# Kernel tuning notes

Hardware: AMD Instinct MI355X
Metric: run time of the kernel (lower is better)

Reference implementation:

```python
import jax, jax.numpy as jnp
import numpy as np

NEG_SLOPE = 0.1
NUM_HEADS = 16
ATT0, ATT1 = 64, 64
FOCUS = 3

def lrelu(x):
    return jnp.where(x >= 0, x, NEG_SLOPE * x)

def adaptive_pool_sum(x, a0, a1):
    # adaptive max pool + adaptive avg pool (exact windows since h%a0==0, w%a1==0)
    B, C, h, w = x.shape
    f0, f1 = h // a0, w // a1
    xr = x.reshape(B, C, a0, f0, a1, f1)
    return xr.max(axis=(3, 5)) + xr.mean(axis=(3, 5))

def upsample_bilinear_ac(x, H, W):
    # bilinear upsample with align_corners=True, matching nn.Upsample
    B, C, h, w = x.shape
    def grid(n_out, n_in):
        t = jnp.arange(n_out, dtype=x.dtype) * ((n_in - 1) / (n_out - 1))
        i0 = jnp.clip(jnp.floor(t).astype(jnp.int32), 0, n_in - 2)
        return i0, t - i0.astype(x.dtype)
    y0, wy = grid(H, h)
    x0, wx = grid(W, w)
    wy = wy[None, None, :, None]
    r = x[:, :, y0, :] * (1 - wy) + x[:, :, y0 + 1, :] * wy
    return r[:, :, :, x0] * (1 - wx) + r[:, :, :, x0 + 1] * wx

def _forward(input1, input2, w_in, b_in, w_v, b_v, scale_param, pos1, pos2):
    B, C, W, H = input1.shape
    N = ATT0 * ATT1
    HD = C // NUM_HEADS
    # conv2input: 1x1 conv dim//2 -> dim (channels differ)
    input2 = jnp.einsum('oc,bchw->bohw', w_in, input2) + b_in[None, :, None, None]
    p1 = adaptive_pool_sum(input1, ATT0, ATT1)  # (B,C,64,64)
    p2 = adaptive_pool_sum(input2, ATT0, ATT1)
    q = p1.reshape(B, C, N).transpose(0, 2, 1)  # (B,N,C)
    t2 = p2.reshape(B, C, N).transpose(0, 2, 1)
    q = lrelu(q + pos1)
    k = lrelu(t2 + pos2)
    v = t2
    scale = jax.nn.softplus(scale_param)  # (1,1,C)
    q = q / scale
    k = k / scale
    def focus(t):
        n = jnp.linalg.norm(t, axis=-1, keepdims=True)
        tp = t ** FOCUS
        return n / jnp.linalg.norm(tp, axis=-1, keepdims=True) * tp
    q = focus(q)
    k = focus(k)
    # head split is head-major: C -> (num_heads, head_dim)
    qh = q.reshape(B, N, NUM_HEADS, HD).transpose(0, 2, 1, 3)  # (B,h,N,d)
    kh = k.reshape(B, N, NUM_HEADS, HD).transpose(0, 2, 1, 3)
    vh = v.reshape(B, N, NUM_HEADS, HD).transpose(0, 2, 1, 3)
    # kv-first linear attention: (k^T N^-.5) @ (v N^-.5) = k^T v / N
    kv = jnp.einsum('bhnd,bhne->bhde', kh, vh) / N  # (B,h,d,d)
    x = jnp.einsum('bhnd,bhde->bhne', qh, kv)       # (B,h,N,d)
    x = x.transpose(0, 1, 3, 2).reshape(B, C, N)     # (B,h,d,N) -> (B,C,N)
    # per-head 1x1 conv + leaky relu on v
    v4 = vh.reshape(B * NUM_HEADS, ATT0, ATT1, HD)
    vc = lrelu(jnp.einsum('bxyd,od->boxy', v4, w_v) + b_v[None, :, None, None])
    x = x + vc.reshape(B, C, N)
    attn = x.reshape(B, C, ATT0, ATT1)
    attn = upsample_bilinear_ac(attn, W, H)
    return jax.nn.sigmoid(attn)

def setup_inputs():
    key = jax.random.key(0)
    ks = jax.random.split(key, 6)
    dim, half, hd, N = 512, 256, 32, ATT0 * ATT1
    return {
        'input1': jax.random.normal(ks[0], (8, dim, 128, 128), jnp.float32),
        'input2': jax.random.normal(ks[1], (8, half, 128, 128), jnp.float32),
        'w_in': jax.random.normal(ks[2], (dim, half), jnp.float32) * 0.05,
        'b_in': jnp.zeros((dim,), jnp.float32),
        'w_v': jax.random.normal(ks[3], (hd, hd), jnp.float32) * 0.1,
        'b_v': jnp.zeros((hd,), jnp.float32),
        'scale_param': jnp.zeros((1, 1, dim), jnp.float32),  # nn.Parameter init zeros
        'pos1': jax.random.normal(ks[4], (1, N, dim), jnp.float32) * 0.02,
        'pos2': jax.random.normal(ks[5], (1, N, dim), jnp.float32) * 0.02,
    }

def reference(input1, input2, w_in, b_in, w_v, b_v, scale_param, pos1, pos2):
    return _forward(input1, input2, w_in, b_in, w_v, b_v, scale_param, pos1, pos2)
```

## Files before the change

### kernel.cpp

```cpp
#include <hip/hip_runtime.h>
#include <math.h>

#define NEG 0.1f

typedef __attribute__((ext_vector_type(8))) short short8;
typedef __attribute__((ext_vector_type(4))) float f32x4;

__device__ __forceinline__ float lrelu(float x){ return x >= 0.f ? x : NEG*x; }

__device__ __forceinline__ unsigned short f2bf(float f){
    unsigned u = __float_as_uint(f);
    return (unsigned short)((u + 0x7FFFu + ((u>>16)&1u)) >> 16);
}
__device__ __forceinline__ unsigned pk2(float lo, float hi){
    return (unsigned)f2bf(lo) | ((unsigned)f2bf(hi) << 16);
}
__device__ __forceinline__ float bflo(unsigned u){ return __uint_as_float(u << 16); }
__device__ __forceinline__ float bfhi(unsigned u){ return __uint_as_float(u & 0xFFFF0000u); }

__global__ __launch_bounds__(256) void k_pool1(const float* __restrict__ in1, unsigned short* __restrict__ p1t){
    __shared__ float s[64*68];
    const int b = blockIdx.z, c0 = blockIdx.y*64, pt = blockIdx.x;
    const int y = pt >> 2, xg = pt & 3;
    const int tid = threadIdx.x;
    #pragma unroll
    for (int it = 0; it < 16; ++it){
        int idx = it*256 + tid;
        int cl = idx >> 6, p = idx & 63;
        int r = p >> 5, xx = p & 31;
        float g = in1[((size_t)(b*512 + c0 + cl)*128 + 2*y + r)*128 + xg*32 + xx];
        s[cl*68 + (xx>>1)*4 + r*2 + (xx&1)] = g;
    }
    __syncthreads();
    const int og = tid & 15, j = tid >> 4;
    float out[4];
    #pragma unroll
    for (int ci = 0; ci < 4; ++ci){
        float4 v = *(const float4*)&s[(og*4+ci)*68 + j*4];
        float m = fmaxf(fmaxf(v.x,v.y), fmaxf(v.z,v.w));
        out[ci] = m + (v.x+v.y+v.z+v.w)*0.25f;
    }
    int n = y*64 + xg*16 + j;
    uint2 d; d.x = pk2(out[0],out[1]); d.y = pk2(out[2],out[3]);
    *(uint2*)&p1t[(size_t)(b*4096 + n)*512 + c0 + og*4] = d;
}

__global__ __launch_bounds__(256) void k_convpool(const float* __restrict__ in2, const float* __restrict__ w_in,
                                                  const float* __restrict__ b_in, unsigned short* __restrict__ p2t){
    __shared__ unsigned As[128*33];
    __shared__ unsigned Bs[128*32];
    const int b = blockIdx.z, o0 = blockIdx.y*128;
    const int y = blockIdx.x >> 1, xg = blockIdx.x & 1;
    const int tid = threadIdx.x;
    const int lane = tid & 63, w = tid >> 6;
    const int col = lane & 15, q = lane >> 4;

    f32x4 acc[2][8];
    #pragma unroll
    for (int mt=0; mt<2; ++mt)
        #pragma unroll
        for (int nt=0; nt<8; ++nt) acc[mt][nt] = (f32x4){0.f,0.f,0.f,0.f};

    const int a_o8 = tid >> 3;
    const int a_kg = tid & 7;
    const int b_c4 = tid & 15, b_r = (tid>>4)&1, b_kg = tid>>5;
    const int b_n = b_r*64 + b_c4*4;

    for (int kb = 0; kb < 4; ++kb){
        __syncthreads();
        #pragma unroll
        for (int pass=0; pass<4; ++pass){
            int o = pass*32 + a_o8;
            const float* src = &w_in[(size_t)(o0+o)*256 + kb*64 + a_kg*8];
            float4 v0 = *(const float4*)src;
            float4 v1 = *(const float4*)(src+4);
            uint4 d;
            d.x = pk2(v0.x, v0.y); d.y = pk2(v0.z, v0.w);
            d.z = pk2(v1.x, v1.y); d.w = pk2(v1.z, v1.w);
            *(uint4*)&As[o*32 + ((a_kg ^ ((o>>1)&7))<<2)] = d;
        }
        float r[8][4];
        #pragma unroll
        for (int kk=0; kk<8; ++kk){
            int k = kb*64 + b_kg*8 + kk;
            float4 v = *(const float4*)&in2[((size_t)(b*256 + k)*128 + 2*y + b_r)*128 + xg*64 + b_c4*4];
            r[kk][0]=v.x; r[kk][1]=v.y; r[kk][2]=v.z; r[kk][3]=v.w;
        }
        #pragma unroll
        for (int i=0; i<4; ++i){
            int n = b_n + i;
            uint4 d;
            d.x = pk2(r[0][i], r[1][i]); d.y = pk2(r[2][i], r[3][i]);
            d.z = pk2(r[4][i], r[5][i]); d.w = pk2(r[6][i], r[7][i]);
            *(uint4*)&Bs[n*32 + ((b_kg ^ ((n>>1)&7))<<2)] = d;
        }
        __syncthreads();
        #pragma unroll
        for (int ks=0; ks<2; ++ks){
            int g = ks*4 + q;
            short8 af[2], bf[8];
            #pragma unroll
            for (int mt=0; mt<2; ++mt){
                int m = w*32 + mt*16 + col;
                af[mt] = *(const short8*)&As[m*32 + ((g ^ ((m>>1)&7))<<2)];
            }
            #pragma unroll
            for (int nt=0; nt<8; ++nt){
                int n = nt*16 + col;
                bf[nt] = *(const short8*)&Bs[n*32 + ((g ^ ((n>>1)&7))<<2)];
            }
            #pragma unroll
            for (int mt=0; mt<2; ++mt)
                #pragma unroll
                for (int nt=0; nt<8; ++nt)
                    acc[mt][nt] = __builtin_amdgcn_mfma_f32_16x16x32_bf16(af[mt], bf[nt], acc[mt][nt], 0,0,0);
        }
    }
    __syncthreads();
    float* outs = (float*)As;
    #pragma unroll
    for (int mt=0; mt<2; ++mt){
        #pragma unroll
        for (int nt=0; nt<4; ++nt){
            #pragma unroll
            for (int reg=0; reg<4; ++reg){
                float a = acc[mt][nt][reg], bb = acc[mt][nt+4][reg];
                float mx = fmaxf(a, bb), sm = a + bb;
                float mx2 = fmaxf(mx, __shfl_xor(mx, 1));
                float sm2 = sm + __shfl_xor(sm, 1);
                if ((lane & 1) == 0){
                    int p = nt*8 + (col>>1);
                    int o = w*32 + mt*16 + q*4 + reg;
                    outs[o*33 + p] = mx2 + sm2*0.25f;
                }
            }
        }
    }
    __syncthreads();
    const int o4 = tid & 31, pp = tid >> 5;
    #pragma unroll
    for (int pass=0; pass<4; ++pass){
        int p = pass*8 + pp;
        int n = y*64 + xg*32 + p;
        float v0 = outs[(o4*4+0)*33 + p] + 2.0f*b_in[o0+o4*4+0];
        float v1 = outs[(o4*4+1)*33 + p] + 2.0f*b_in[o0+o4*4+1];
        float v2 = outs[(o4*4+2)*33 + p] + 2.0f*b_in[o0+o4*4+2];
        float v3 = outs[(o4*4+3)*33 + p] + 2.0f*b_in[o0+o4*4+3];
        uint2 d; d.x = pk2(v0,v1); d.y = pk2(v2,v3);
        *(uint2*)&p2t[(size_t)(b*4096 + n)*512 + o0 + o4*4] = d;
    }
}

__global__ __launch_bounds__(256) void k_rows(unsigned* __restrict__ p1u, const unsigned* __restrict__ p2u,
                                              const float* __restrict__ pos1, const float* __restrict__ pos2,
                                              const float* __restrict__ scale_param, unsigned* __restrict__ kfu){
    const int n = blockIdx.x, b = blockIdx.y;
    const int tid = threadIdx.x;
    const size_t baseu = (size_t)(b*4096 + n)*256;
    const int c0 = tid*2;
    __shared__ float red[4][4];
    unsigned u1 = p1u[baseu + tid];
    unsigned u2 = p2u[baseu + tid];
    float2 po1 = *(const float2*)&pos1[n*512 + c0];
    float2 po2 = *(const float2*)&pos2[n*512 + c0];
    float2 scv = *(const float2*)&scale_param[c0];
    float qv[2], kv_[2];
    float pq2=0.f, pq6=0.f, pk2_=0.f, pk6=0.f;
    {
        float sp0 = scv.x, sp1 = scv.y;
        float inv0 = 1.0f/(fmaxf(sp0,0.f) + log1pf(expf(-fabsf(sp0))));
        float inv1 = 1.0f/(fmaxf(sp1,0.f) + log1pf(expf(-fabsf(sp1))));
        float q0 = lrelu(bflo(u1) + po1.x) * inv0;
        float q1 = lrelu(bfhi(u1) + po1.y) * inv1;
        float k0 = lrelu(bflo(u2) + po2.x) * inv0;
        float k1 = lrelu(bfhi(u2) + po2.y) * inv1;
        qv[0]=q0; qv[1]=q1; kv_[0]=k0; kv_[1]=k1;
        float a;
        a = q0*q0; pq2 += a; pq6 += a*a*a;
        a = q1*q1; pq2 += a; pq6 += a*a*a;
        a = k0*k0; pk2_ += a; pk6 += a*a*a;
        a = k1*k1; pk2_ += a; pk6 += a*a*a;
    }
    #pragma unroll
    for (int off = 32; off > 0; off >>= 1){
        pq2 += __shfl_xor(pq2, off);
        pq6 += __shfl_xor(pq6, off);
        pk2_ += __shfl_xor(pk2_, off);
        pk6 += __shfl_xor(pk6, off);
    }
    int wave = tid >> 6;
    if ((tid & 63) == 0){ red[wave][0]=pq2; red[wave][1]=pq6; red[wave][2]=pk2_; red[wave][3]=pk6; }
    __syncthreads();
    float sq2 = red[0][0]+red[1][0]+red[2][0]+red[3][0];
    float sq6 = red[0][1]+red[1][1]+red[2][1]+red[3][1];
    float sk2 = red[0][2]+red[1][2]+red[2][2]+red[3][2];
    float sk6 = red[0][3]+red[1][3]+red[2][3]+red[3][3];
    float fq = sqrtf(sq2/sq6);
    float fk = sqrtf(sk2/sk6);
    p1u[baseu + tid] = pk2(qv[0]*qv[0]*qv[0]*fq, qv[1]*qv[1]*qv[1]*fq);
    kfu[baseu + tid] = pk2(kv_[0]*kv_[0]*kv_[0]*fk, kv_[1]*kv_[1]*kv_[1]*fk);
}

__global__ __launch_bounds__(256) void k_kv(const unsigned* __restrict__ kfu, const unsigned* __restrict__ p2u,
                                            float* __restrict__ kv){
    __shared__ float ks[512], vs[512];
    const int nc = blockIdx.x, h = blockIdx.y, b = blockIdx.z;
    const int tid = threadIdx.x;
    const int d = tid >> 3, eb = (tid & 7) * 4;
    const int nn_ld = tid >> 4, cp = tid & 15;
    float acc[4] = {0.f,0.f,0.f,0.f};
    for (int s = 0; s < 16; ++s){
        int n0 = nc*256 + s*16;
        size_t g = (size_t)(b*4096 + n0 + nn_ld)*256 + h*16 + cp;
        unsigned ku = kfu[g], vu = p2u[g];
        ks[nn_ld*32 + cp*2]   = bflo(ku);
        ks[nn_ld*32 + cp*2+1] = bfhi(ku);
        vs[nn_ld*32 + cp*2]   = bflo(vu);
        vs[nn_ld*32 + cp*2+1] = bfhi(vu);
        __syncthreads();
        #pragma unroll
        for (int nn = 0; nn < 16; ++nn){
            float kd = ks[nn*32 + d];
            float4 vv = *(const float4*)&vs[nn*32 + eb];
            acc[0] += kd*vv.x; acc[1] += kd*vv.y; acc[2] += kd*vv.z; acc[3] += kd*vv.w;
        }
        __syncthreads();
    }
    float* dst = &kv[((size_t)(b*16 + h)*32 + d)*32 + eb];
    const float sc = 1.0f/4096.0f;
    atomicAdd(dst+0, acc[0]*sc);
    atomicAdd(dst+1, acc[1]*sc);
    atomicAdd(dst+2, acc[2]*sc);
    atomicAdd(dst+3, acc[3]*sc);
}

__global__ __launch_bounds__(256) void k_attn(const unsigned* __restrict__ qfu, const unsigned* __restrict__ p2u,
                                              const float* __restrict__ kv, const float* __restrict__ w_v,
                                              const float* __restrict__ b_v, unsigned short* __restrict__ attn){
    __shared__ float kvs[1024];
    __shared__ float wvsT[32*36];
    __shared__ float qsl[64*32];
    __shared__ float vsl[64*32];
    __shared__ float to[32*66];
    const int nt = blockIdx.x, h = blockIdx.y, b = blockIdx.z;
    const int tid = threadIdx.x;
    #pragma unroll
    for (int it = 0; it < 4; ++it){
        int i = it*256 + tid;
        kvs[i] = kv[(size_t)(b*16 + h)*1024 + i];
        int e_ = i >> 5, d_ = i & 31;
        wvsT[d_*36 + e_] = w_v[e_*32 + d_];
    }
    #pragma unroll
    for (int it = 0; it < 4; ++it){
        int i = it*256 + tid;
        int nn = i >> 4, cp = i & 15;
        size_t g = (size_t)(b*4096 + nt*64 + nn)*256 + h*16 + cp;
        unsigned qu = qfu[g], vu = p2u[g];
        qsl[nn*32 + cp*2]   = bflo(qu);
        qsl[nn*32 + cp*2+1] = bfhi(qu);
        vsl[nn*32 + cp*2]   = bflo(vu);
        vsl[nn*32 + cp*2+1] = bfhi(vu);
    }
    __syncthreads();
    const int e0 = (tid & 7)*4, ng = tid >> 3;
    float4 bv = make_float4(b_v[e0], b_v[e0+1], b_v[e0+2], b_v[e0+3]);
    #pragma unroll
    for (int half = 0; half < 2; ++half){
        int nn = ng + half*32;
        float xa[4] = {0.f,0.f,0.f,0.f}, va[4] = {0.f,0.f,0.f,0.f};
        #pragma unroll
        for (int dq = 0; dq < 8; ++dq){
            float4 q4 = *(const float4*)&qsl[nn*32 + dq*4];
            float4 v4 = *(const float4*)&vsl[nn*32 + dq*4];
            float qarr[4] = {q4.x,q4.y,q4.z,q4.w};
            float varr[4] = {v4.x,v4.y,v4.z,v4.w};
            #pragma unroll
            for (int l = 0; l < 4; ++l){
                int d = dq*4 + l;
                float4 kvv = *(const float4*)&kvs[d*32 + e0];
                float4 wvv = *(const float4*)&wvsT[d*36 + e0];
                xa[0] += qarr[l]*kvv.x; xa[1] += qarr[l]*kvv.y; xa[2] += qarr[l]*kvv.z; xa[3] += qarr[l]*kvv.w;
                va[0] += varr[l]*wvv.x; va[1] += varr[l]*wvv.y; va[2] += varr[l]*wvv.z; va[3] += varr[l]*wvv.w;
            }
        }
        to[(e0+0)*66 + nn] = xa[0] + lrelu(va[0] + bv.x);
        to[(e0+1)*66 + nn] = xa[1] + lrelu(va[1] + bv.y);
        to[(e0+2)*66 + nn] = xa[2] + lrelu(va[2] + bv.z);
        to[(e0+3)*66 + nn] = xa[3] + lrelu(va[3] + bv.w);
    }
    __syncthreads();
    const int cc = tid >> 3, n0 = (tid & 7)*8;
    uint4 d;
    d.x = pk2(to[cc*66+n0+0], to[cc*66+n0+1]);
    d.y = pk2(to[cc*66+n0+2], to[cc*66+n0+3]);
    d.z = pk2(to[cc*66+n0+4], to[cc*66+n0+5]);
    d.w = pk2(to[cc*66+n0+6], to[cc*66+n0+7]);
    *(uint4*)&attn[((size_t)(b*512) + h*32 + cc)*4096 + nt*64 + n0] = d;
}

__global__ __launch_bounds__(256) void k_up(const unsigned* __restrict__ attn_u, float* __restrict__ out){
    __shared__ float sA[18*65];
    const int qy = blockIdx.x;
    const int bc = blockIdx.y;
    const int tid = threadIdx.x;
    const int ybase = (qy*32*63)/127;
    const size_t sb = (size_t)bc*2048;
    for (int i = tid; i < 576; i += 256){
        int r = i >> 5, cu = i & 31;
        int ridx = ybase + r; if (ridx > 63) ridx = 63;
        unsigned u = attn_u[sb + ridx*32 + cu];
        sA[r*65 + cu*2]   = bflo(u);
        sA[r*65 + cu*2+1] = bfhi(u);
    }
    __syncthreads();
    const float rr = 63.0f/127.0f;
    const int ro = tid >> 3, cbase = tid & 7;
    const int yo = qy*32 + ro;
    float ty = yo * rr;
    int y0 = (int)ty; y0 = y0 > 62 ? 62 : y0;
    float wy = ty - (float)y0;
    const float* ra = &sA[(y0 - ybase)*65];
    const float* rb = ra + 65;
    float* orow = &out[((size_t)bc*128 + yo)*128];
    #pragma unroll
    for (int t = 0; t < 4; ++t){
        int xo0 = (cbase + t*8)*4;
        float4 o;
        float* op = (float*)&o;
        #pragma unroll
        for (int j = 0; j < 4; ++j){
            int xo = xo0 + j;
            float tx = xo * rr;
            int x0 = (int)tx; x0 = x0 > 62 ? 62 : x0;
            float wx = tx - (float)x0;
            float a00 = ra[x0], a01 = ra[x0+1];
            float a10 = rb[x0], a11 = rb[x0+1];
            float v = (a00*(1.f-wy) + a10*wy)*(1.f-wx) + (a01*(1.f-wy) + a11*wy)*wx;
            op[j] = 1.0f/(1.0f + expf(-v));
        }
        *(float4*)&orow[xo0] = o;
    }
}

extern "C" void kernel_launch(void* const* d_in, const int* in_sizes, int n_in,
                              void* d_out, int out_size, void* d_ws, size_t ws_size,
                              hipStream_t stream){
    const float* in1  = (const float*)d_in[0];
    const float* in2  = (const float*)d_in[1];
    const float* w_in = (const float*)d_in[2];
    const float* b_in = (const float*)d_in[3];
    const float* w_v  = (const float*)d_in[4];
    const float* b_v  = (const float*)d_in[5];
    const float* scp  = (const float*)d_in[6];
    const float* pos1 = (const float*)d_in[7];
    const float* pos2 = (const float*)d_in[8];
    float* out = (float*)d_out;
    char* ws  = (char*)d_ws;

    const size_t PBYTES = (size_t)8*4096*512*2;
    unsigned short* p1t  = (unsigned short*)ws;
    unsigned short* p2t  = (unsigned short*)(ws + PBYTES);
    unsigned short* kfoc = (unsigned short*)(ws + 2*PBYTES);
    float*          kvb  = (float*)(ws + 3*PBYTES);

    hipMemsetAsync(kvb, 0, (size_t)8*16*32*32*sizeof(float), stream);
    k_pool1   <<<dim3(256,8,8), 256, 0, stream>>>(in1, p1t);
    k_convpool<<<dim3(128,4,8), 256, 0, stream>>>(in2, w_in, b_in, p2t);
    k_rows    <<<dim3(4096,8),  256, 0, stream>>>((unsigned*)p1t, (const unsigned*)p2t, pos1, pos2, scp, (unsigned*)kfoc);
    k_kv      <<<dim3(16,16,8), 256, 0, stream>>>((const unsigned*)kfoc, (const unsigned*)p2t, kvb);
    k_attn    <<<dim3(64,16,8), 256, 0, stream>>>((const unsigned*)p1t, (const unsigned*)p2t, kvb, w_v, b_v, kfoc);
    k_up      <<<dim3(4,4096),  256, 0, stream>>>((const unsigned*)kfoc, out);
}
```

Measured before the change: 843.7 us.

## Rework pool1, row normalisation, kv reduction and pre-convert conv weights to bf16

Several kernels change at once. k_pool1 drops the shared-memory transpose and reads float2 pairs directly, writing 8 channels per thread. A new k_wprep kernel converts w_in to bf16 once, so k_convpool loads packed weights instead of converting them in every block. k_rows handles two rows per block with 4 channels per thread, and k_kv stages its whole 256-row chunk in shared memory as bf16 with a single sync. bf16 packing now uses the HIP intrinsic. The aim is fewer blocks, fewer barriers and wider memory accesses, at the cost of an extra launch and less coalesced pool reads.

```diff
diff --git a/kernel.cpp b/kernel.cpp
--- a/kernel.cpp
+++ b/kernel.cpp
@@ -1,4 +1,5 @@
 #include <hip/hip_runtime.h>
+#include <hip/hip_bf16.h>
 #include <math.h>
 
 #define NEG 0.1f
@@ -8,44 +9,48 @@
 
 __device__ __forceinline__ float lrelu(float x){ return x >= 0.f ? x : NEG*x; }
 
-__device__ __forceinline__ unsigned short f2bf(float f){
-    unsigned u = __float_as_uint(f);
-    return (unsigned short)((u + 0x7FFFu + ((u>>16)&1u)) >> 16);
-}
 __device__ __forceinline__ unsigned pk2(float lo, float hi){
-    return (unsigned)f2bf(lo) | ((unsigned)f2bf(hi) << 16);
+    __hip_bfloat162 h = __float22bfloat162_rn(make_float2(lo, hi));
+    union { __hip_bfloat162 h2; unsigned u; } cv; cv.h2 = h;
+    return cv.u;
 }
 __device__ __forceinline__ float bflo(unsigned u){ return __uint_as_float(u << 16); }
 __device__ __forceinline__ float bfhi(unsigned u){ return __uint_as_float(u & 0xFFFF0000u); }
 
-__global__ __launch_bounds__(256) void k_pool1(const float* __restrict__ in1, unsigned short* __restrict__ p1t){
-    __shared__ float s[64*68];
-    const int b = blockIdx.z, c0 = blockIdx.y*64, pt = blockIdx.x;
-    const int y = pt >> 2, xg = pt & 3;
-    const int tid = threadIdx.x;
-    #pragma unroll
-    for (int it = 0; it < 16; ++it){
-        int idx = it*256 + tid;
-        int cl = idx >> 6, p = idx & 63;
-        int r = p >> 5, xx = p & 31;
-        float g = in1[((size_t)(b*512 + c0 + cl)*128 + 2*y + r)*128 + xg*32 + xx];
-        s[cl*68 + (xx>>1)*4 + r*2 + (xx&1)] = g;
-    }
-    __syncthreads();
-    const int og = tid & 15, j = tid >> 4;
-    float out[4];
-    #pragma unroll
-    for (int ci = 0; ci < 4; ++ci){
-        float4 v = *(const float4*)&s[(og*4+ci)*68 + j*4];
-        float m = fmaxf(fmaxf(v.x,v.y), fmaxf(v.z,v.w));
-        out[ci] = m + (v.x+v.y+v.z+v.w)*0.25f;
-    }
-    int n = y*64 + xg*16 + j;
-    uint2 d; d.x = pk2(out[0],out[1]); d.y = pk2(out[2],out[3]);
-    *(uint2*)&p1t[(size_t)(b*4096 + n)*512 + c0 + og*4] = d;
-}
-
-__global__ __launch_bounds__(256) void k_convpool(const float* __restrict__ in2, const float* __restrict__ w_in,
+__global__ __launch_bounds__(256) void k_wprep(const float* __restrict__ w_in, unsigned* __restrict__ wbf_u){
+    int idx8 = (blockIdx.x*256 + threadIdx.x)*8;
+    float4 v0 = *(const float4*)&w_in[idx8];
+    float4 v1 = *(const float4*)&w_in[idx8+4];
+    uint4 d;
+    d.x = pk2(v0.x, v0.y); d.y = pk2(v0.z, v0.w);
+    d.z = pk2(v1.x, v1.y); d.w = pk2(v1.z, v1.w);
+    *(uint4*)&wbf_u[idx8>>1] = d;
+}
+
+__global__ __launch_bounds__(256) void k_pool1(const float* __restrict__ in1, unsigned* __restrict__ p1u){
+    const int y = blockIdx.x, cg = blockIdx.y, b = blockIdx.z;
+    const int tid = threadIdx.x;
+    const int x = tid & 63, w = tid >> 6;
+    const int cbase = cg*32 + w*8;
+    const float2* iv = (const float2*)in1;
+    float out[8];
+    #pragma unroll
+    for (int j = 0; j < 8; ++j){
+        int c = cbase + j;
+        size_t r0 = (size_t)(b*512 + c)*8192 + (2*y)*64 + x;
+        float2 a = iv[r0];
+        float2 bb = iv[r0 + 64];
+        float m = fmaxf(fmaxf(a.x,a.y), fmaxf(bb.x,bb.y));
+        out[j] = m + (a.x+a.y+bb.x+bb.y)*0.25f;
+    }
+    uint4 d;
+    d.x = pk2(out[0],out[1]); d.y = pk2(out[2],out[3]);
+    d.z = pk2(out[4],out[5]); d.w = pk2(out[6],out[7]);
+    int n = y*64 + x;
+    *(uint4*)&p1u[(size_t)(b*4096 + n)*256 + cg*16 + w*4] = d;
+}
+
+__global__ __launch_bounds__(256) void k_convpool(const float* __restrict__ in2, const unsigned* __restrict__ wbf_u,
                                                   const float* __restrict__ b_in, unsigned short* __restrict__ p2t){
     __shared__ unsigned As[128*33];
     __shared__ unsigned Bs[128*32];
@@ -71,12 +76,7 @@
         #pragma unroll
         for (int pass=0; pass<4; ++pass){
             int o = pass*32 + a_o8;
-            const float* src = &w_in[(size_t)(o0+o)*256 + kb*64 + a_kg*8];
-            float4 v0 = *(const float4*)src;
-            float4 v1 = *(const float4*)(src+4);
-            uint4 d;
-            d.x = pk2(v0.x, v0.y); d.y = pk2(v0.z, v0.w);
-            d.z = pk2(v1.x, v1.y); d.w = pk2(v1.z, v1.w);
+            uint4 d = *(const uint4*)&wbf_u[((size_t)(o0+o)*256 + kb*64 + a_kg*8) >> 1];
             *(uint4*)&As[o*32 + ((a_kg ^ ((o>>1)&7))<<2)] = d;
         }
         float r[8][4];
@@ -154,32 +154,37 @@
 __global__ __launch_bounds__(256) void k_rows(unsigned* __restrict__ p1u, const unsigned* __restrict__ p2u,
                                               const float* __restrict__ pos1, const float* __restrict__ pos2,
                                               const float* __restrict__ scale_param, unsigned* __restrict__ kfu){
-    const int n = blockIdx.x, b = blockIdx.y;
-    const int tid = threadIdx.x;
-    const size_t baseu = (size_t)(b*4096 + n)*256;
-    const int c0 = tid*2;
+    const int b = blockIdx.y;
+    const int tid = threadIdx.x;
+    const int half = tid >> 7, t = tid & 127;
+    const int n = blockIdx.x*2 + half;
+    const int c0 = t*4;
+    const size_t base2 = (size_t)(b*4096 + n)*128;
     __shared__ float red[4][4];
-    unsigned u1 = p1u[baseu + tid];
-    unsigned u2 = p2u[baseu + tid];
-    float2 po1 = *(const float2*)&pos1[n*512 + c0];
-    float2 po2 = *(const float2*)&pos2[n*512 + c0];
-    float2 scv = *(const float2*)&scale_param[c0];
-    float qv[2], kv_[2];
+    uint2 u1 = *(const uint2*)&p1u[base2*2 + t*2];
+    uint2 u2 = *(const uint2*)&p2u[base2*2 + t*2];
+    float4 po1 = *(const float4*)&pos1[n*512 + c0];
+    float4 po2 = *(const float4*)&pos2[n*512 + c0];
+    float4 scv = *(const float4*)&scale_param[c0];
+    float qv[4], kv_[4];
     float pq2=0.f, pq6=0.f, pk2_=0.f, pk6=0.f;
     {
-        float sp0 = scv.x, sp1 = scv.y;
-        float inv0 = 1.0f/(fmaxf(sp0,0.f) + log1pf(expf(-fabsf(sp0))));
-        float inv1 = 1.0f/(fmaxf(sp1,0.f) + log1pf(expf(-fabsf(sp1))));
-        float q0 = lrelu(bflo(u1) + po1.x) * inv0;
-        float q1 = lrelu(bfhi(u1) + po1.y) * inv1;
-        float k0 = lrelu(bflo(u2) + po2.x) * inv0;
-        float k1 = lrelu(bfhi(u2) + po2.y) * inv1;
-        qv[0]=q0; qv[1]=q1; kv_[0]=k0; kv_[1]=k1;
-        float a;
-        a = q0*q0; pq2 += a; pq6 += a*a*a;
-        a = q1*q1; pq2 += a; pq6 += a*a*a;
-        a = k0*k0; pk2_ += a; pk6 += a*a*a;
-        a = k1*k1; pk2_ += a; pk6 += a*a*a;
+        float p1a[4] = {bflo(u1.x), bfhi(u1.x), bflo(u1.y), bfhi(u1.y)};
+        float p2a[4] = {bflo(u2.x), bfhi(u2.x), bflo(u2.y), bfhi(u2.y)};
+        float poa1[4] = {po1.x,po1.y,po1.z,po1.w};
+        float poa2[4] = {po2.x,po2.y,po2.z,po2.w};
+        float sca[4] = {scv.x,scv.y,scv.z,scv.w};
+        #pragma unroll
+        for (int j = 0; j < 4; ++j){
+            float sp = sca[j];
+            float inv = 1.0f/(fmaxf(sp,0.f) + log1pf(expf(-fabsf(sp))));
+            float qq = lrelu(p1a[j] + poa1[j]) * inv;
+            float kk = lrelu(p2a[j] + poa2[j]) * inv;
+            qv[j]=qq; kv_[j]=kk;
+            float a;
+            a = qq*qq; pq2 += a; pq6 += a*a*a;
+            a = kk*kk; pk2_ += a; pk6 += a*a*a;
+        }
     }
     #pragma unroll
     for (int off = 32; off > 0; off >>= 1){
@@ -191,42 +196,47 @@
     int wave = tid >> 6;
     if ((tid & 63) == 0){ red[wave][0]=pq2; red[wave][1]=pq6; red[wave][2]=pk2_; red[wave][3]=pk6; }
     __syncthreads();
-    float sq2 = red[0][0]+red[1][0]+red[2][0]+red[3][0];
-    float sq6 = red[0][1]+red[1][1]+red[2][1]+red[3][1];
-    float sk2 = red[0][2]+red[1][2]+red[2][2]+red[3][2];
-    float sk6 = red[0][3]+red[1][3]+red[2][3]+red[3][3];
+    float sq2 = red[2*half][0]+red[2*half+1][0];
+    float sq6 = red[2*half][1]+red[2*half+1][1];
+    float sk2 = red[2*half][2]+red[2*half+1][2];
+    float sk6 = red[2*half][3]+red[2*half+1][3];
     float fq = sqrtf(sq2/sq6);
     float fk = sqrtf(sk2/sk6);
-    p1u[baseu + tid] = pk2(qv[0]*qv[0]*qv[0]*fq, qv[1]*qv[1]*qv[1]*fq);
-    kfu[baseu + tid] = pk2(kv_[0]*kv_[0]*kv_[0]*fk, kv_[1]*kv_[1]*kv_[1]*fk);
+    uint2 dq, dk;
+    dq.x = pk2(qv[0]*qv[0]*qv[0]*fq, qv[1]*qv[1]*qv[1]*fq);
+    dq.y = pk2(qv[2]*qv[2]*qv[2]*fq, qv[3]*qv[3]*qv[3]*fq);
+    dk.x = pk2(kv_[0]*kv_[0]*kv_[0]*fk, kv_[1]*kv_[1]*kv_[1]*fk);
+    dk.y = pk2(kv_[2]*kv_[2]*kv_[2]*fk, kv_[3]*kv_[3]*kv_[3]*fk);
+    *(uint2*)&p1u[base2*2 + t*2] = dq;
+    *(uint2*)&kfu[base2*2 + t*2] = dk;
 }
 
 __global__ __launch_bounds__(256) void k_kv(const unsigned* __restrict__ kfu, const unsigned* __restrict__ p2u,
                                             float* __restrict__ kv){
-    __shared__ float ks[512], vs[512];
+    __shared__ unsigned ksu[4096], vsu[4096];
     const int nc = blockIdx.x, h = blockIdx.y, b = blockIdx.z;
     const int tid = threadIdx.x;
-    const int d = tid >> 3, eb = (tid & 7) * 4;
-    const int nn_ld = tid >> 4, cp = tid & 15;
+    #pragma unroll
+    for (int it = 0; it < 16; ++it){
+        int i = it*256 + tid;
+        int n = i >> 4, u = i & 15;
+        size_t g = (size_t)(b*4096 + nc*256 + n)*256 + h*16 + u;
+        ksu[i] = kfu[g];
+        vsu[i] = p2u[g];
+    }
+    __syncthreads();
+    const int d = tid >> 3, e2 = (tid & 7)*2;
+    const unsigned kmaskhi = (d & 1) ? 1u : 0u;
     float acc[4] = {0.f,0.f,0.f,0.f};
-    for (int s = 0; s < 16; ++s){
-        int n0 = nc*256 + s*16;
-        size_t g = (size_t)(b*4096 + n0 + nn_ld)*256 + h*16 + cp;
-        unsigned ku = kfu[g], vu = p2u[g];
-        ks[nn_ld*32 + cp*2]   = bflo(ku);
-        ks[nn_ld*32 + cp*2+1] = bfhi(ku);
-        vs[nn_ld*32 + cp*2]   = bflo(vu);
-        vs[nn_ld*32 + cp*2+1] = bfhi(vu);
-        __syncthreads();
-        #pragma unroll
-        for (int nn = 0; nn < 16; ++nn){
-            float kd = ks[nn*32 + d];
-            float4 vv = *(const float4*)&vs[nn*32 + eb];
-            acc[0] += kd*vv.x; acc[1] += kd*vv.y; acc[2] += kd*vv.z; acc[3] += kd*vv.w;
-        }
-        __syncthreads();
-    }
-    float* dst = &kv[((size_t)(b*16 + h)*32 + d)*32 + eb];
+    #pragma unroll 8
+    for (int n = 0; n < 256; ++n){
+        unsigned ku = ksu[n*16 + (d>>1)];
+        float kd = kmaskhi ? bfhi(ku) : bflo(ku);
+        uint2 vv = *(const uint2*)&vsu[n*16 + e2];
+        acc[0] += kd*bflo(vv.x); acc[1] += kd*bfhi(vv.x);
+        acc[2] += kd*bflo(vv.y); acc[3] += kd*bfhi(vv.y);
+    }
+    float* dst = &kv[((size_t)(b*16 + h)*32 + d)*32 + (tid&7)*4];
     const float sc = 1.0f/4096.0f;
     atomicAdd(dst+0, acc[0]*sc);
     atomicAdd(dst+1, acc[1]*sc);
@@ -363,11 +373,13 @@
     unsigned short* p2t  = (unsigned short*)(ws + PBYTES);
     unsigned short* kfoc = (unsigned short*)(ws + 2*PBYTES);
     float*          kvb  = (float*)(ws + 3*PBYTES);
+    unsigned*       wbf  = (unsigned*)(ws + 3*PBYTES + (size_t)8*16*32*32*4);
 
     hipMemsetAsync(kvb, 0, (size_t)8*16*32*32*sizeof(float), stream);
-    k_pool1   <<<dim3(256,8,8), 256, 0, stream>>>(in1, p1t);
-    k_convpool<<<dim3(128,4,8), 256, 0, stream>>>(in2, w_in, b_in, p2t);
-    k_rows    <<<dim3(4096,8),  256, 0, stream>>>((unsigned*)p1t, (const unsigned*)p2t, pos1, pos2, scp, (unsigned*)kfoc);
+    k_wprep   <<<64,            256, 0, stream>>>(w_in, wbf);
+    k_pool1   <<<dim3(64,16,8), 256, 0, stream>>>(in1, (unsigned*)p1t);
+    k_convpool<<<dim3(128,4,8), 256, 0, stream>>>(in2, wbf, b_in, p2t);
+    k_rows    <<<dim3(2048,8),  256, 0, stream>>>((unsigned*)p1t, (const unsigned*)p2t, pos1, pos2, scp, (unsigned*)kfoc);
     k_kv      <<<dim3(16,16,8), 256, 0, stream>>>((const unsigned*)kfoc, (const unsigned*)p2t, kvb);
     k_attn    <<<dim3(64,16,8), 256, 0, stream>>>((const unsigned*)p1t, (const unsigned*)p2t, kvb, w_v, b_v, kfoc);
     k_up      <<<dim3(4,4096),  256, 0, stream>>>((const unsigned*)kfoc, out);
```

Result: faster. 813.6 us (-3.6%).
